# Performance work log

Hardware: AMD Instinct MI355X
Metric: run time of the kernel (lower is better)

The kernel has to match this reference:

```python
import jax, jax.numpy as jnp
import numpy as np

B, T, F, H = 4096, 128, 64, 32
SCALE = 0.05  # small init so relu-LSTM doesn't blow up over 128 steps


def setup_inputs() -> dict:
    key = jax.random.key(0)
    ks = jax.random.split(key, 7)
    return {
        "x": jax.random.normal(ks[0], (B, T, F), jnp.float32),
        "We": jax.random.normal(ks[1], (F, 4 * H), jnp.float32) * SCALE,
        "Ue": jax.random.normal(ks[2], (H, 4 * H), jnp.float32) * SCALE,
        "be": jnp.zeros((4 * H,), jnp.float32),
        "Wd": jax.random.normal(ks[3], (H, 4 * H), jnp.float32) * SCALE,
        "Ud": jax.random.normal(ks[4], (H, 4 * H), jnp.float32) * SCALE,
        "bd": jnp.zeros((4 * H,), jnp.float32),
        "Wout": jax.random.normal(ks[5], (H, F), jnp.float32) * SCALE,
        "bout": jnp.zeros((F,), jnp.float32),
    }


def _lstm_relu(x, W, U, b):
    """Keras LSTM with activation='relu', recurrent_activation='sigmoid'.
    x: [B,T,D]. Returns (h_T [B,H], h_seq [B,T,H]). Gate order: i,f,c,o."""
    Bx = x.shape[0]
    Hh = U.shape[0]
    xz = jnp.einsum('btd,dg->btg', x, W) + b  # precompute input projections

    def step(carry, zt):
        h, c = carry
        z = zt + h @ U
        i, f, g, o = jnp.split(z, 4, axis=-1)
        i = jax.nn.sigmoid(i)
        f = jax.nn.sigmoid(f)
        g = jax.nn.relu(g)
        o = jax.nn.sigmoid(o)
        c = f * c + i * g
        h = o * jax.nn.relu(c)
        return (h, c), h

    h0 = jnp.zeros((Bx, Hh), x.dtype)
    (hT, _), hs = jax.lax.scan(step, (h0, h0), jnp.swapaxes(xz, 0, 1))
    return hT, jnp.swapaxes(hs, 0, 1)


def reference(x, We, Ue, be, Wd, Ud, bd, Wout, bout):
    # Encoder: LSTM(32, relu, return_sequences=False) -> RepeatVector(T)
    hT, _ = _lstm_relu(x, We, Ue, be)                      # [B,H]
    z = jnp.broadcast_to(hT[:, None, :], (x.shape[0], x.shape[1], hT.shape[-1]))
    # Decoder: LSTM(32, relu, return_sequences=True) -> TimeDistributed(Dense(F))
    _, hs = _lstm_relu(z, Wd, Ud, bd)                      # [B,T,H]
    return jnp.einsum('bth,hf->btf', hs, Wout) + bout      # [B,T,F]
```

## Files before the change

### kernel.cpp

```cpp
#include <hip/hip_runtime.h>
#include <hip/hip_bf16.h>

#define B_ 4096
#define T_ 128
#define F_ 64
#define H_ 32
#define G_ 128

using short8 = __attribute__((ext_vector_type(8))) short;
using f32x4  = __attribute__((ext_vector_type(4))) float;
using uint2v = __attribute__((ext_vector_type(2))) unsigned int;
using uint4v = __attribute__((ext_vector_type(4))) unsigned int;

#define MFMA16(Af, Bf, Cf) __builtin_amdgcn_mfma_f32_16x16x32_bf16((Af), (Bf), (Cf), 0, 0, 0)

__device__ __forceinline__ float sigmoid_f(float z) {
    return __builtin_amdgcn_rcpf(1.0f + __expf(-z));
}
__device__ __forceinline__ unsigned short bfb(float f) {
    return __builtin_bit_cast(unsigned short, __float2bfloat16(f));
}
__device__ __forceinline__ unsigned int pk(float a, float b) {
    return (unsigned int)bfb(a) | ((unsigned int)bfb(b) << 16);
}

extern "C" __global__ __launch_bounds__(128, 1)
void lstm_ae(const float* __restrict__ x,
             const float* __restrict__ We,
             const float* __restrict__ Ue,
             const float* __restrict__ be,
             const float* __restrict__ Wd,
             const float* __restrict__ Ud,
             const float* __restrict__ bd,
             const float* __restrict__ Wout,
             const float* __restrict__ bout,
             float* __restrict__ out)
{
    const int lane = threadIdx.x & 63;
    const int w    = threadIdx.x >> 6;
    const int g    = lane >> 4;
    const int c    = lane & 15;
    const int b0   = blockIdx.x << 4;

    __shared__ __align__(16) unsigned int hx[2][16][18];

    short8 weF[4][2];
    short8 ueF[4];
    f32x4  beC[4];
#pragma unroll
    for (int q = 0; q < 4; ++q) {
        const int n = 2 * q + w;
#pragma unroll
        for (int kc = 0; kc < 2; ++kc)
#pragma unroll
            for (int i = 0; i < 8; ++i)
                weF[q][kc][i] = (short)bfb(We[(kc * 32 + 8 * g + i) * G_ + 16 * n + c]);
#pragma unroll
        for (int i = 0; i < 8; ++i)
            ueF[q][i] = (short)bfb(Ue[(4 * g + (i & 3) + 16 * (i >> 2)) * G_ + 16 * n + c]);
        beC[q] = *(const f32x4*)(be + 16 * n + 4 * g);
    }

    const float* xr = x + (size_t)(b0 + c) * (T_ * F_);
    const int xo = 8 * g;

    short8 hfrag = (short8)0;
    float cs[4];
#pragma unroll
    for (int r = 0; r < 4; ++r) cs[r] = 0.f;

    f32x4 xa = *(const f32x4*)(xr + xo);
    f32x4 xb = *(const f32x4*)(xr + xo + 4);
    f32x4 xc = *(const f32x4*)(xr + 32 + xo);
    f32x4 xd = *(const f32x4*)(xr + 36 + xo);

#pragma unroll 1
    for (int t = 0; t < T_; ++t) {
        short8 xf0, xf1;
#pragma unroll
        for (int i = 0; i < 4; ++i) {
            xf0[i]     = (short)bfb(xa[i]);
            xf0[4 + i] = (short)bfb(xb[i]);
            xf1[i]     = (short)bfb(xc[i]);
            xf1[4 + i] = (short)bfb(xd[i]);
        }
        if (t + 1 < T_) {
            const float* xn = xr + (t + 1) * F_;
            xa = *(const f32x4*)(xn + xo);
            xb = *(const f32x4*)(xn + xo + 4);
            xc = *(const f32x4*)(xn + 32 + xo);
            xd = *(const f32x4*)(xn + 36 + xo);
        }

        f32x4 acc[4];
#pragma unroll
        for (int q = 0; q < 4; ++q) {
            acc[q] = MFMA16(weF[q][0], xf0, beC[q]);
            acc[q] = MFMA16(weF[q][1], xf1, acc[q]);
            acc[q] = MFMA16(ueF[q], hfrag, acc[q]);
        }

        float hv[4];
#pragma unroll
        for (int r = 0; r < 4; ++r) {
            float iv = sigmoid_f(acc[0][r]);
            float fv = sigmoid_f(acc[1][r]);
            float gv = fmaxf(acc[2][r], 0.f);
            float ov = sigmoid_f(acc[3][r]);
            float cc = fmaf(fv, cs[r], iv * gv);
            cs[r] = cc;
            hv[r] = ov * fmaxf(cc, 0.f);
        }
        uint2v own; own.x = pk(hv[0], hv[1]); own.y = pk(hv[2], hv[3]);
        *(uint2v*)&hx[t & 1][c][8 * w + 2 * g] = own;
        __syncthreads();
        uint2v oth = *(const uint2v*)&hx[t & 1][c][8 * (1 - w) + 2 * g];
        uint4v hb;
        hb.x = w ? oth.x : own.x;
        hb.y = w ? oth.y : own.y;
        hb.z = w ? own.x : oth.x;
        hb.w = w ? own.y : oth.y;
        hfrag = __builtin_bit_cast(short8, hb);
    }

    short8 udF[4], woF[2];
    f32x4  zd[4], boC[2];
    {
        short8 wdF[4];
#pragma unroll
        for (int q = 0; q < 4; ++q) {
            const int n = 2 * q + w;
#pragma unroll
            for (int i = 0; i < 8; ++i) {
                const int pr = 4 * g + (i & 3) + 16 * (i >> 2);
                wdF[q][i] = (short)bfb(Wd[pr * G_ + 16 * n + c]);
                udF[q][i] = (short)bfb(Ud[pr * G_ + 16 * n + c]);
            }
        }
#pragma unroll
        for (int mi = 0; mi < 2; ++mi) {
            const int m = 2 * w + mi;
#pragma unroll
            for (int i = 0; i < 8; ++i)
                woF[mi][i] = (short)bfb(Wout[(4 * g + (i & 3) + 16 * (i >> 2)) * F_ + 16 * m + c]);
            float v = bout[16 * m + c];
            f32x4 tb; tb[0] = v; tb[1] = v; tb[2] = v; tb[3] = v;
            boC[mi] = tb;
        }
#pragma unroll
        for (int q = 0; q < 4; ++q) {
            f32x4 tb = *(const f32x4*)(bd + 16 * (2 * q + w) + 4 * g);
            zd[q] = MFMA16(wdF[q], hfrag, tb);
        }
    }

    hfrag = (short8)0;
#pragma unroll
    for (int r = 0; r < 4; ++r) cs[r] = 0.f;

    float* ob[4];
#pragma unroll
    for (int r = 0; r < 4; ++r)
        ob[r] = out + (size_t)(b0 + 4 * g + r) * (T_ * F_) + c;

#pragma unroll 1
    for (int t = 0; t < T_; ++t) {
        f32x4 acc[4];
#pragma unroll
        for (int q = 0; q < 4; ++q)
            acc[q] = MFMA16(udF[q], hfrag, zd[q]);

        float hv[4];
#pragma unroll
        for (int r = 0; r < 4; ++r) {
            float iv = sigmoid_f(acc[0][r]);
            float fv = sigmoid_f(acc[1][r]);
            float gv = fmaxf(acc[2][r], 0.f);
            float ov = sigmoid_f(acc[3][r]);
            float cc = fmaf(fv, cs[r], iv * gv);
            cs[r] = cc;
            hv[r] = ov * fmaxf(cc, 0.f);
        }
        uint2v own; own.x = pk(hv[0], hv[1]); own.y = pk(hv[2], hv[3]);
        *(uint2v*)&hx[t & 1][c][8 * w + 2 * g] = own;
        __syncthreads();
        uint2v oth = *(const uint2v*)&hx[t & 1][c][8 * (1 - w) + 2 * g];
        uint4v hb;
        hb.x = w ? oth.x : own.x;
        hb.y = w ? oth.y : own.y;
        hb.z = w ? own.x : oth.x;
        hb.w = w ? own.y : oth.y;
        hfrag = __builtin_bit_cast(short8, hb);

#pragma unroll
        for (int mi = 0; mi < 2; ++mi) {
            f32x4 oac = MFMA16(hfrag, woF[mi], boC[mi]);
            const int m = 2 * w + mi;
#pragma unroll
            for (int r = 0; r < 4; ++r)
                ob[r][t * F_ + 16 * m] = oac[r];
        }
    }
}

extern "C" void kernel_launch(void* const* d_in, const int* in_sizes, int n_in,
                              void* d_out, int out_size, void* d_ws, size_t ws_size,
                              hipStream_t stream) {
    (void)in_sizes; (void)n_in; (void)d_ws; (void)ws_size; (void)out_size;
    const float* x    = (const float*)d_in[0];
    const float* We   = (const float*)d_in[1];
    const float* Ue   = (const float*)d_in[2];
    const float* be   = (const float*)d_in[3];
    const float* Wd   = (const float*)d_in[4];
    const float* Ud   = (const float*)d_in[5];
    const float* bd   = (const float*)d_in[6];
    const float* Wout = (const float*)d_in[7];
    const float* bout = (const float*)d_in[8];
    float* out = (float*)d_out;

    dim3 grid(B_ / 16), block(128);
    hipLaunchKernelGGL(lstm_ae, grid, block, 0, stream,
                       x, We, Ue, be, Wd, Ud, bd, Wout, bout, out);
}
```

Before: 345.6 us.

## Split work into consumer and producer waves to pipeline input projection

The block grows from two to four waves. Two producer waves compute the encoder input projection for the next timestep, or the decoder output projection, and pass results through double-buffered shared memory. The two consumer waves keep only the recurrent MFMA and the gate math on the serial critical path. This is meant to take x loads, conversions and output stores off the recurrence chain. The cost is extra LDS traffic, and every step still needs a block-wide barrier across four waves.

Result: slower. 365.5 us (+5.8%).

```diff
diff --git a/kernel.cpp b/kernel.cpp
--- a/kernel.cpp
+++ b/kernel.cpp
@@ -24,7 +24,7 @@
     return (unsigned int)bfb(a) | ((unsigned int)bfb(b) << 16);
 }
 
-extern "C" __global__ __launch_bounds__(128, 1)
+extern "C" __global__ __launch_bounds__(256, 1)
 void lstm_ae(const float* __restrict__ x,
              const float* __restrict__ We,
              const float* __restrict__ Ue,
@@ -36,100 +36,153 @@
              const float* __restrict__ bout,
              float* __restrict__ out)
 {
-    const int lane = threadIdx.x & 63;
-    const int w    = threadIdx.x >> 6;
-    const int g    = lane >> 4;
-    const int c    = lane & 15;
-    const int b0   = blockIdx.x << 4;
-
-    __shared__ __align__(16) unsigned int hx[2][16][18];
-
+    const int  lane = threadIdx.x & 63;
+    const int  w    = threadIdx.x >> 6;
+    const bool con  = (w < 2);
+    const int  rw   = w & 1;
+    const int  g    = lane >> 4;
+    const int  c    = lane & 15;
+    const int  b0   = blockIdx.x << 4;
+
+    __shared__ __align__(16) unsigned int hx[2][16 * 18];
+    __shared__ __align__(16) f32x4 zxbuf[2][8][64];
+
+    short8 ueF[4];
     short8 weF[4][2];
-    short8 ueF[4];
     f32x4  beC[4];
-#pragma unroll
-    for (int q = 0; q < 4; ++q) {
-        const int n = 2 * q + w;
-#pragma unroll
-        for (int kc = 0; kc < 2; ++kc)
-#pragma unroll
-            for (int i = 0; i < 8; ++i)
-                weF[q][kc][i] = (short)bfb(We[(kc * 32 + 8 * g + i) * G_ + 16 * n + c]);
-#pragma unroll
-        for (int i = 0; i < 8; ++i)
-            ueF[q][i] = (short)bfb(Ue[(4 * g + (i & 3) + 16 * (i >> 2)) * G_ + 16 * n + c]);
-        beC[q] = *(const f32x4*)(be + 16 * n + 4 * g);
-    }
+    short8 hfrag = (short8)0;
+    float  cs[4] = {0.f, 0.f, 0.f, 0.f};
+    f32x4  zxC[4];
+    f32x4  xa, xb, xc, xd;
 
     const float* xr = x + (size_t)(b0 + c) * (T_ * F_);
     const int xo = 8 * g;
 
-    short8 hfrag = (short8)0;
-    float cs[4];
-#pragma unroll
-    for (int r = 0; r < 4; ++r) cs[r] = 0.f;
-
-    f32x4 xa = *(const f32x4*)(xr + xo);
-    f32x4 xb = *(const f32x4*)(xr + xo + 4);
-    f32x4 xc = *(const f32x4*)(xr + 32 + xo);
-    f32x4 xd = *(const f32x4*)(xr + 36 + xo);
+#define CVTX(xf0, xf1)                                   \
+    {                                                    \
+        _Pragma("unroll")                                \
+        for (int i = 0; i < 4; ++i) {                    \
+            xf0[i]     = (short)bfb(xa[i]);              \
+            xf0[4 + i] = (short)bfb(xb[i]);              \
+            xf1[i]     = (short)bfb(xc[i]);              \
+            xf1[4 + i] = (short)bfb(xd[i]);              \
+        }                                                \
+    }
+
+#define GATES4(ACC, OWN)                                 \
+    {                                                    \
+        float hv[4];                                     \
+        _Pragma("unroll")                                \
+        for (int r = 0; r < 4; ++r) {                    \
+            float iv = sigmoid_f(ACC[0][r]);             \
+            float fv = sigmoid_f(ACC[1][r]);             \
+            float gv = fmaxf(ACC[2][r], 0.f);            \
+            float ov = sigmoid_f(ACC[3][r]);             \
+            float cc = fmaf(fv, cs[r], iv * gv);         \
+            cs[r] = cc;                                  \
+            hv[r] = ov * fmaxf(cc, 0.f);                 \
+        }                                                \
+        OWN.x = pk(hv[0], hv[1]);                        \
+        OWN.y = pk(hv[2], hv[3]);                        \
+    }
+
+    if (con) {
+#pragma unroll
+        for (int q = 0; q < 4; ++q) {
+            const int n = 2 * q + rw;
+#pragma unroll
+            for (int i = 0; i < 8; ++i)
+                ueF[q][i] = (short)bfb(Ue[(4 * g + (i & 3) + 16 * (i >> 2)) * G_ + 16 * n + c]);
+        }
+    } else {
+#pragma unroll
+        for (int q = 0; q < 4; ++q) {
+            const int n = 2 * q + rw;
+#pragma unroll
+            for (int kc = 0; kc < 2; ++kc)
+#pragma unroll
+                for (int i = 0; i < 8; ++i)
+                    weF[q][kc][i] = (short)bfb(We[(kc * 32 + 8 * g + i) * G_ + 16 * n + c]);
+            beC[q] = *(const f32x4*)(be + 16 * n + 4 * g);
+        }
+        xa = *(const f32x4*)(xr + xo);
+        xb = *(const f32x4*)(xr + xo + 4);
+        xc = *(const f32x4*)(xr + 32 + xo);
+        xd = *(const f32x4*)(xr + 36 + xo);
+        short8 xf0, xf1;
+        CVTX(xf0, xf1)
+#pragma unroll
+        for (int q = 0; q < 4; ++q) {
+            f32x4 z = MFMA16(weF[q][0], xf0, beC[q]);
+            z = MFMA16(weF[q][1], xf1, z);
+            zxbuf[0][2 * q + rw][lane] = z;
+        }
+        const float* xn = xr + F_;
+        xa = *(const f32x4*)(xn + xo);
+        xb = *(const f32x4*)(xn + xo + 4);
+        xc = *(const f32x4*)(xn + 32 + xo);
+        xd = *(const f32x4*)(xn + 36 + xo);
+    }
+    __syncthreads();
+    if (con) {
+#pragma unroll
+        for (int q = 0; q < 4; ++q) zxC[q] = zxbuf[0][2 * q + rw][lane];
+    }
 
 #pragma unroll 1
     for (int t = 0; t < T_; ++t) {
-        short8 xf0, xf1;
-#pragma unroll
-        for (int i = 0; i < 4; ++i) {
-            xf0[i]     = (short)bfb(xa[i]);
-            xf0[4 + i] = (short)bfb(xb[i]);
-            xf1[i]     = (short)bfb(xc[i]);
-            xf1[4 + i] = (short)bfb(xd[i]);
-        }
-        if (t + 1 < T_) {
-            const float* xn = xr + (t + 1) * F_;
-            xa = *(const f32x4*)(xn + xo);
-            xb = *(const f32x4*)(xn + xo + 4);
-            xc = *(const f32x4*)(xn + 32 + xo);
-            xd = *(const f32x4*)(xn + 36 + xo);
-        }
-
-        f32x4 acc[4];
-#pragma unroll
-        for (int q = 0; q < 4; ++q) {
-            acc[q] = MFMA16(weF[q][0], xf0, beC[q]);
-            acc[q] = MFMA16(weF[q][1], xf1, acc[q]);
-            acc[q] = MFMA16(ueF[q], hfrag, acc[q]);
-        }
-
-        float hv[4];
-#pragma unroll
-        for (int r = 0; r < 4; ++r) {
-            float iv = sigmoid_f(acc[0][r]);
-            float fv = sigmoid_f(acc[1][r]);
-            float gv = fmaxf(acc[2][r], 0.f);
-            float ov = sigmoid_f(acc[3][r]);
-            float cc = fmaf(fv, cs[r], iv * gv);
-            cs[r] = cc;
-            hv[r] = ov * fmaxf(cc, 0.f);
-        }
-        uint2v own; own.x = pk(hv[0], hv[1]); own.y = pk(hv[2], hv[3]);
-        *(uint2v*)&hx[t & 1][c][8 * w + 2 * g] = own;
+        uint2v own;
+        if (con) {
+            f32x4 acc[4];
+#pragma unroll
+            for (int q = 0; q < 4; ++q)
+                acc[q] = MFMA16(ueF[q], hfrag, zxC[q]);
+            GATES4(acc, own)
+            *(uint2v*)&hx[t & 1][c * 18 + 8 * rw + 2 * g] = own;
+        } else if (t + 1 < T_) {
+            short8 xf0, xf1;
+            CVTX(xf0, xf1)
+            if (t + 2 < T_) {
+                const float* xn = xr + (t + 2) * F_;
+                xa = *(const f32x4*)(xn + xo);
+                xb = *(const f32x4*)(xn + xo + 4);
+                xc = *(const f32x4*)(xn + 32 + xo);
+                xd = *(const f32x4*)(xn + 36 + xo);
+            }
+#pragma unroll
+            for (int q = 0; q < 4; ++q) {
+                f32x4 z = MFMA16(weF[q][0], xf0, beC[q]);
+                z = MFMA16(weF[q][1], xf1, z);
+                zxbuf[(t + 1) & 1][2 * q + rw][lane] = z;
+            }
+        }
         __syncthreads();
-        uint2v oth = *(const uint2v*)&hx[t & 1][c][8 * (1 - w) + 2 * g];
-        uint4v hb;
-        hb.x = w ? oth.x : own.x;
-        hb.y = w ? oth.y : own.y;
-        hb.z = w ? own.x : oth.x;
-        hb.w = w ? own.y : oth.y;
-        hfrag = __builtin_bit_cast(short8, hb);
-    }
-
-    short8 udF[4], woF[2];
-    f32x4  zd[4], boC[2];
-    {
+        if (con) {
+            uint2v oth = *(const uint2v*)&hx[t & 1][c * 18 + 8 * (1 - rw) + 2 * g];
+            uint4v hb;
+            hb.x = rw ? oth.x : own.x;
+            hb.y = rw ? oth.y : own.y;
+            hb.z = rw ? own.x : oth.x;
+            hb.w = rw ? own.y : oth.y;
+            hfrag = __builtin_bit_cast(short8, hb);
+            if (t + 1 < T_) {
+#pragma unroll
+                for (int q = 0; q < 4; ++q)
+                    zxC[q] = zxbuf[(t + 1) & 1][2 * q + rw][lane];
+            }
+        }
+    }
+
+    short8 udF[4];
+    f32x4  zd[4];
+    short8 woF[2];
+    f32x4  boC[2];
+    float* ob[4];
+    if (con) {
         short8 wdF[4];
 #pragma unroll
         for (int q = 0; q < 4; ++q) {
-            const int n = 2 * q + w;
+            const int n = 2 * q + rw;
 #pragma unroll
             for (int i = 0; i < 8; ++i) {
                 const int pr = 4 * g + (i & 3) + 16 * (i >> 2);
@@ -138,67 +191,61 @@
             }
         }
 #pragma unroll
+        for (int q = 0; q < 4; ++q) {
+            f32x4 tb = *(const f32x4*)(bd + 16 * (2 * q + rw) + 4 * g);
+            zd[q] = MFMA16(wdF[q], hfrag, tb);
+        }
+        hfrag = (short8)0;
+#pragma unroll
+        for (int r = 0; r < 4; ++r) cs[r] = 0.f;
+    } else {
+#pragma unroll
         for (int mi = 0; mi < 2; ++mi) {
-            const int m = 2 * w + mi;
+            const int m = 2 * rw + mi;
 #pragma unroll
             for (int i = 0; i < 8; ++i)
                 woF[mi][i] = (short)bfb(Wout[(4 * g + (i & 3) + 16 * (i >> 2)) * F_ + 16 * m + c]);
             float v = bout[16 * m + c];
-            f32x4 tb; tb[0] = v; tb[1] = v; tb[2] = v; tb[3] = v;
-            boC[mi] = tb;
-        }
-#pragma unroll
-        for (int q = 0; q < 4; ++q) {
-            f32x4 tb = *(const f32x4*)(bd + 16 * (2 * q + w) + 4 * g);
-            zd[q] = MFMA16(wdF[q], hfrag, tb);
-        }
-    }
-
-    hfrag = (short8)0;
-#pragma unroll
-    for (int r = 0; r < 4; ++r) cs[r] = 0.f;
-
-    float* ob[4];
-#pragma unroll
-    for (int r = 0; r < 4; ++r)
-        ob[r] = out + (size_t)(b0 + 4 * g + r) * (T_ * F_) + c;
+            boC[mi][0] = v; boC[mi][1] = v; boC[mi][2] = v; boC[mi][3] = v;
+        }
+#pragma unroll
+        for (int r = 0; r < 4; ++r)
+            ob[r] = out + (size_t)(b0 + 4 * g + r) * (T_ * F_) + c;
+    }
 
 #pragma unroll 1
     for (int t = 0; t < T_; ++t) {
-        f32x4 acc[4];
-#pragma unroll
-        for (int q = 0; q < 4; ++q)
-            acc[q] = MFMA16(udF[q], hfrag, zd[q]);
-
-        float hv[4];
-#pragma unroll
-        for (int r = 0; r < 4; ++r) {
-            float iv = sigmoid_f(acc[0][r]);
-            float fv = sigmoid_f(acc[1][r]);
-            float gv = fmaxf(acc[2][r], 0.f);
-            float ov = sigmoid_f(acc[3][r]);
-            float cc = fmaf(fv, cs[r], iv * gv);
-            cs[r] = cc;
-            hv[r] = ov * fmaxf(cc, 0.f);
-        }
-        uint2v own; own.x = pk(hv[0], hv[1]); own.y = pk(hv[2], hv[3]);
-        *(uint2v*)&hx[t & 1][c][8 * w + 2 * g] = own;
+        uint2v own;
+        if (con) {
+            f32x4 acc[4];
+#pragma unroll
+            for (int q = 0; q < 4; ++q)
+                acc[q] = MFMA16(udF[q], hfrag, zd[q]);
+            GATES4(acc, own)
+            *(uint2v*)&hx[t & 1][c * 18 + 8 * rw + 2 * g] = own;
+        }
         __syncthreads();
-        uint2v oth = *(const uint2v*)&hx[t & 1][c][8 * (1 - w) + 2 * g];
-        uint4v hb;
-        hb.x = w ? oth.x : own.x;
-        hb.y = w ? oth.y : own.y;
-        hb.z = w ? own.x : oth.x;
-        hb.w = w ? own.y : oth.y;
-        hfrag = __builtin_bit_cast(short8, hb);
-
-#pragma unroll
-        for (int mi = 0; mi < 2; ++mi) {
-            f32x4 oac = MFMA16(hfrag, woF[mi], boC[mi]);
-            const int m = 2 * w + mi;
-#pragma unroll
-            for (int r = 0; r < 4; ++r)
-                ob[r][t * F_ + 16 * m] = oac[r];
+        if (con) {
+            uint2v oth = *(const uint2v*)&hx[t & 1][c * 18 + 8 * (1 - rw) + 2 * g];
+            uint4v hb;
+            hb.x = rw ? oth.x : own.x;
+            hb.y = rw ? oth.y : own.y;
+            hb.z = rw ? own.x : oth.x;
+            hb.w = rw ? own.y : oth.y;
+            hfrag = __builtin_bit_cast(short8, hb);
+        } else {
+            uint2v ha = *(const uint2v*)&hx[t & 1][c * 18 + 2 * g];
+            uint2v hz = *(const uint2v*)&hx[t & 1][c * 18 + 8 + 2 * g];
+            uint4v u; u.x = ha.x; u.y = ha.y; u.z = hz.x; u.w = hz.y;
+            short8 hA = __builtin_bit_cast(short8, u);
+#pragma unroll
+            for (int mi = 0; mi < 2; ++mi) {
+                f32x4 oac = MFMA16(hA, woF[mi], boC[mi]);
+                const int m = 2 * rw + mi;
+#pragma unroll
+                for (int r = 0; r < 4; ++r)
+                    ob[r][t * F_ + 16 * m] = oac[r];
+            }
         }
     }
 }
@@ -218,7 +265,7 @@
     const float* bout = (const float*)d_in[8];
     float* out = (float*)d_out;
 
-    dim3 grid(B_ / 16), block(128);
+    dim3 grid(B_ / 16), block(256);
     hipLaunchKernelGGL(lstm_ae, grid, block, 0, stream,
                        x, We, Ue, be, Wd, Ud, bd, Wout, bout, out);
 }
```
